# Kernel optimization log

Hardware: AMD Instinct MI355X
Metric: run time of the kernel (lower is better)

The kernel has to match this reference:

```python
import jax, jax.numpy as jnp
import numpy as np

IMAGE_W = 1024; IMAGE_H = 1024
STRIDES = (8, 16, 32, 64, 128)
TOP_N = 1000; MIN_SCORE = 0.01; NMS_THR = 0.6; MAX_DET = 100
BATCH = 16; NUM_CLASSES = 80


def setup_inputs():
    keys = jax.random.split(jax.random.key(0), 3 * len(STRIDES))
    inp = {}
    for l, s in enumerate(STRIDES):
        H, W = IMAGE_H // s, IMAGE_W // s
        inp[f"cls_head_{l}"] = jax.random.normal(keys[3 * l], (BATCH, H, W, NUM_CLASSES), jnp.float32)
        inp[f"reg_head_{l}"] = jax.random.normal(keys[3 * l + 1], (BATCH, H, W, 4), jnp.float32)
        inp[f"center_head_{l}"] = jax.random.normal(keys[3 * l + 2], (BATCH, H, W, 1), jnp.float32)
        xs = (jnp.arange(W, dtype=jnp.float32) + 0.5) * s
        ys = (jnp.arange(H, dtype=jnp.float32) + 0.5) * s
        gx, gy = jnp.meshgrid(xs, ys)  # each [H, W]
        pos = jnp.stack([gx, gy], axis=-1)  # [H, W, 2] = (ctr_x, ctr_y)
        inp[f"position_{l}"] = jnp.broadcast_to(pos, (BATCH, H, W, 2))
    return inp


def _decode_levels(cls_heads, reg_heads, center_heads, positions):
    S, C, R, P = [], [], [], []
    for cls, reg, ctr, pos in zip(cls_heads, reg_heads, center_heads, positions):
        B = cls.shape[0]
        cls = jax.nn.sigmoid(cls).reshape(B, -1, cls.shape[-1])  # [B,N,C]
        reg = jnp.exp(reg).reshape(B, -1, 4)
        ctr = jax.nn.sigmoid(ctr).reshape(B, -1)
        pos = pos.reshape(B, -1, 2)
        scores = jnp.sqrt(jnp.max(cls, axis=2) * ctr)  # sqrt(cls_max * centerness)
        classes = jnp.argmax(cls, axis=2)
        if scores.shape[1] >= TOP_N:
            scores, idx = jax.lax.top_k(scores, TOP_N)
            classes = jnp.take_along_axis(classes, idx, axis=1)
            reg = jnp.take_along_axis(reg, idx[:, :, None], axis=1)
            pos = jnp.take_along_axis(pos, idx[:, :, None], axis=1)
        S.append(scores); C.append(classes); R.append(reg); P.append(pos)
    return (jnp.concatenate(S, 1), jnp.concatenate(C, 1),
            jnp.concatenate(R, 1), jnp.concatenate(P, 1))


def _nms_keep(boxes, valid, iou_thr):
    # greedy class-agnostic NMS on score-descending boxes [N,4]
    N = boxes.shape[0]
    x1, y1, x2, y2 = boxes[:, 0], boxes[:, 1], boxes[:, 2], boxes[:, 3]
    areas = (x2 - x1) * (y2 - y1)
    idx = jnp.arange(N)

    def body(i, suppressed):
        keep_i = valid[i] & ~suppressed[i]
        xx1 = jnp.maximum(x1[i], x1); yy1 = jnp.maximum(y1[i], y1)
        xx2 = jnp.minimum(x2[i], x2); yy2 = jnp.minimum(y2[i], y2)
        inter = jnp.maximum(xx2 - xx1, 0.0) * jnp.maximum(yy2 - yy1, 0.0)
        iou = inter / (areas[i] + areas - inter)
        return suppressed | (keep_i & (iou > iou_thr) & (idx > i))

    suppressed = jax.lax.fori_loop(0, N, body, jnp.zeros((N,), bool))
    return valid & ~suppressed


def _per_image(scores, classes, reg, pos):
    xy_min = pos - reg[:, 0:2]
    xy_max = pos + reg[:, 2:4]
    boxes = jnp.concatenate([xy_min, xy_max], axis=1).astype(jnp.int32)  # trunc like .int()
    boxes = jnp.stack([jnp.maximum(boxes[:, 0], 0),
                       jnp.maximum(boxes[:, 1], 0),
                       jnp.minimum(boxes[:, 2], IMAGE_W - 1),
                       jnp.minimum(boxes[:, 3], IMAGE_H - 1)], axis=1).astype(jnp.float32)
    valid = scores > MIN_SCORE
    order = jnp.argsort(jnp.where(valid, -scores, jnp.inf))  # valid, score-descending first
    sb, ss = boxes[order], scores[order]
    sc, sv = classes[order].astype(jnp.float32), valid[order]
    kept = _nms_keep(sb, sv, NMS_THR)
    rank = jnp.cumsum(kept) - 1
    slot = jnp.where(kept, jnp.minimum(rank, MAX_DET), MAX_DET)  # overflow -> scratch slot
    out_s = jnp.full((MAX_DET + 1,), -1.0, jnp.float32).at[slot].set(jnp.where(kept, ss, -1.0))[:MAX_DET]
    out_c = jnp.full((MAX_DET + 1,), -1.0, jnp.float32).at[slot].set(jnp.where(kept, sc, -1.0))[:MAX_DET]
    out_b = jnp.full((MAX_DET + 1, 4), -1.0, jnp.float32).at[slot].set(jnp.where(kept[:, None], sb, -1.0))[:MAX_DET]
    return out_s, out_c, out_b


def _forward(cls_heads, reg_heads, center_heads, positions):
    s, c, r, p = _decode_levels(cls_heads, reg_heads, center_heads, positions)
    return jax.vmap(_per_image)(s, c, r, p)


def reference(cls_head_0, reg_head_0, center_head_0, position_0,
              cls_head_1, reg_head_1, center_head_1, position_1,
              cls_head_2, reg_head_2, center_head_2, position_2,
              cls_head_3, reg_head_3, center_head_3, position_3,
              cls_head_4, reg_head_4, center_head_4, position_4):
    cls_heads = [cls_head_0, cls_head_1, cls_head_2, cls_head_3, cls_head_4]
    reg_heads = [reg_head_0, reg_head_1, reg_head_2, reg_head_3, reg_head_4]
    center_heads = [center_head_0, center_head_1, center_head_2, center_head_3, center_head_4]
    positions = [position_0, position_1, position_2, position_3, position_4]
    return _forward(cls_heads, reg_heads, center_heads, positions)
```

## Files before the change

kernel.cpp:

```cpp
#include <hip/hip_runtime.h>
#include <stdint.h>

#define BATCH 16
#define NCLS 80
#define NPOS 21824
#define POOLN 3320
#define MAXDET 100

#define CAP0 4096
#define CAP1 2432
#define CAP2 1024
#define C34 320
#define CAP34 320
#define SEG1 (CAP0)
#define SEG2 (CAP0 + CAP1)
#define SEG3 (CAP0 + CAP1 + CAP2)
#define CAPTOT (SEG3 + CAP34)

#define DEC_BPI 341
#define GATHER_BPI 16
#define GATHER_CHUNK 1344
#define POS_BPI 13

#define NBINS 4096
#define HIST_TPI 11

__device__ const int d_lvl_off[5] = {0, 16384, 20480, 21504, 21760};
__device__ const int d_lvl_hw[5]  = {16384, 4096, 1024, 256, 64};

struct Ptrs { const float* p[20]; };

__device__ __forceinline__ void map_lvl(int r, int& level, int& hw) {
  if      (r < 16384) { level = 0; hw = r; }
  else if (r < 20480) { level = 1; hw = r - 16384; }
  else if (r < 21504) { level = 2; hw = r - 20480; }
  else if (r < 21760) { level = 3; hw = r - 21504; }
  else                { level = 4; hw = r - 21760; }
}


__global__ __launch_bounds__(256) void decode_kernel(Ptrs args, uint4* __restrict__ dec,
                                                     unsigned long long* __restrict__ gbuf,
                                                     int* __restrict__ gcnt,
                                                     unsigned* __restrict__ sbuf) {
  __shared__ float2 sm[1280];
  int b  = blockIdx.x / DEC_BPI;
  int bb = blockIdx.x - b * DEC_BPI;
  int t = threadIdx.x;
  if (bb == 0 && t < 3) gcnt[b * 3 + t] = 0;

  int flat0 = bb * 64;
  int level, hw0;
  map_lvl(flat0, level, hw0);
  int HW = d_lvl_hw[level];

  const float* cls = args.p[level * 4 + 0];
  const float* reg = args.p[level * 4 + 1];
  const float* ctr = args.p[level * 4 + 2];
  const float* pos = args.p[level * 4 + 3];

  const float4* c4 = (const float4*)(cls + ((long)b * HW + hw0) * NCLS);
#pragma unroll
  for (int w = 0; w < 5; ++w) {
    int f = t + 256 * w;
    float4 v = c4[f];
    int q = f % 20;
    float m = -1e30f; int am = 4 * q;
    if (v.x > m) { m = v.x; am = 4 * q + 0; }
    if (v.y > m) { m = v.y; am = 4 * q + 1; }
    if (v.z > m) { m = v.z; am = 4 * q + 2; }
    if (v.w > m) { m = v.w; am = 4 * q + 3; }
    sm[f] = make_float2(m, __int_as_float(am));
  }
  __syncthreads();

  int aoff = t >> 2, r = t & 3;
  int base = aoff * 20 + 5 * r;
  float2 c0 = sm[base];
  float m = c0.x; int am = __float_as_int(c0.y);
#pragma unroll
  for (int i = 1; i < 5; ++i) {
    float2 cc = sm[base + i];
    int oa = __float_as_int(cc.y);
    if (cc.x > m || (cc.x == m && oa < am)) { m = cc.x; am = oa; }
  }
#pragma unroll
  for (int d = 1; d <= 2; d <<= 1) {
    float om = __shfl_xor(m, d, 64);
    int   oa = __shfl_xor(am, d, 64);
    if (om > m || (om == m && oa < am)) { m = om; am = oa; }
  }

  if (r == 0) {
    int hw = hw0 + aoff;
    long abase = (long)b * HW + hw;
    float4 rg = *(const float4*)(reg + abase * 4);
    float  ct = ctr[abase];
    float2 ps = ((const float2*)pos)[abase];

    float e0 = expf(rg.x), e1 = expf(rg.y), e2 = expf(rg.z), e3 = expf(rg.w);
    int x1 = (int)(ps.x - e0);
    int y1 = (int)(ps.y - e1);
    int x2 = (int)(ps.x + e2);
    int y2 = (int)(ps.y + e3);
    x1 = max(x1, 0); y1 = max(y1, 0);
    x2 = min(x2, 1023); y2 = min(y2, 1023);

    float sigm = 1.0f / (1.0f + expf(-m));
    float sigc = 1.0f / (1.0f + expf(-ct));
    float score = sqrtf(sigm * sigc);

    uint4 e;
    e.x = __float_as_uint(score);
    e.y = (unsigned)am;
    e.z = (unsigned)(x1 & 0xFFFF) | ((unsigned)y1 << 16);
    e.w = (unsigned)(x2 & 0xFFFF) | ((unsigned)y2 << 16);
    dec[b * NPOS + flat0 + aoff] = e;

    unsigned nsb = ~e.x;
    sbuf[b * NPOS + flat0 + aoff] = nsb;
    if (level >= 3) {
      unsigned long long key =
          ((unsigned long long)nsb << 32) | (unsigned)((level << 20) | hw);
      gbuf[(size_t)b * CAPTOT + SEG3 + ((level == 3) ? hw : 256 + hw)] = key;
    }
  }
}

__global__ __launch_bounds__(256) void hist_kernel(const unsigned* __restrict__ sbuf,
                                                   unsigned* __restrict__ ghist) {
  __shared__ unsigned h[NBINS];
  int img = blockIdx.x / HIST_TPI, task = blockIdx.x % HIST_TPI;
  int level, start, n;
  if      (task < 8)  { level = 0; start = task * 2048;       n = 2048; }
  else if (task < 10) { level = 1; start = (task - 8) * 2048; n = 2048; }
  else                { level = 2; start = 0;                 n = 1024; }
  int tid = threadIdx.x;

  for (int i = tid; i < NBINS; i += 256) h[i] = 0;
  __syncthreads();
  const unsigned* base = sbuf + img * NPOS + d_lvl_off[level] + start;
  for (int i = tid; i < n; i += 256)
    atomicAdd(&h[base[i] >> 20], 1u);
  __syncthreads();
  unsigned* gh = ghist + (unsigned)(img * 3 + level) * NBINS;
  for (int i = tid; i < NBINS; i += 256) {
    unsigned v = h[i];
    if (v) atomicAdd(&gh[i], v);
  }
}

__global__ __launch_bounds__(256) void cutoff_kernel(const unsigned* __restrict__ ghist,
                                                     int* __restrict__ bcut) {
  __shared__ unsigned wpart[4];
  __shared__ int shB;
  int img = blockIdx.x / 3, level = blockIdx.x % 3;
  const unsigned* h = ghist + (unsigned)(img * 3 + level) * NBINS;
  int tid = threadIdx.x, lane = tid & 63, wv = tid >> 6;

  unsigned hl[16];
  unsigned s = 0;
#pragma unroll
  for (int k = 0; k < 16; ++k) { hl[k] = h[16 * tid + k]; s += hl[k]; }
  unsigned incl = s;
  for (int d = 1; d < 64; d <<= 1) {
    unsigned v = __shfl_up(incl, d, 64);
    if (lane >= d) incl += v;
  }
  if (lane == 63) wpart[wv] = incl;
  __syncthreads();
  unsigned woff = 0;
  for (int w = 0; w < wv; ++w) woff += wpart[w];
  unsigned excl = woff + incl - s;
  if (excl < 1000u && excl + s >= 1000u) {
    unsigned cum = excl; int B = NBINS - 1;
#pragma unroll
    for (int k = 0; k < 16; ++k) {
      cum += hl[k];
      if (cum >= 1000u) { B = 16 * tid + k; break; }
    }
    shB = B;
  }
  __syncthreads();
  if (tid == 0) bcut[img * 3 + level] = shB;
}

__global__ __launch_bounds__(256) void gather_kernel(const unsigned* __restrict__ sbuf,
                                                     const int* __restrict__ bcut,
                                                     unsigned long long* __restrict__ gbuf,
                                                     int* __restrict__ gcnt) {
  int img = blockIdx.x / GATHER_BPI, bb = blockIdx.x % GATHER_BPI;
  int tid = threadIdx.x, lane = tid & 63;
  int start = bb * GATHER_CHUNK;
  int b0 = bcut[img * 3 + 0], b1 = bcut[img * 3 + 1], b2 = bcut[img * 3 + 2];
  unsigned long long* gb = gbuf + (size_t)img * CAPTOT;

  for (int j = start + tid; j < start + GATHER_CHUNK; j += 256) {
    int level, hw;
    map_lvl(j, level, hw);
    unsigned nsb = sbuf[img * NPOS + j];
    bool sel = (int)(nsb >> 20) <= ((level == 0) ? b0 : (level == 1) ? b1 : b2);
    unsigned long long msk = __ballot(sel);
    if (msk) {
      int nsel = __popcll(msk);
      int bas = 0;
      if (lane == 0) bas = atomicAdd(&gcnt[img * 3 + level], nsel);
      bas = __shfl(bas, 0, 64);
      if (sel) {
        int p = bas + __popcll(msk & ((1ULL << lane) - 1ULL));
        int cap   = (level == 0) ? CAP0 : (level == 1) ? CAP1 : CAP2;
        int sbase = (level == 0) ? 0    : (level == 1) ? SEG1 : SEG2;
        unsigned long long key =
            ((unsigned long long)nsb << 32) | (unsigned)((level << 20) | hw);
        if (p < cap) gb[sbase + p] = key;
      }
    }
  }
}

#define SWQ(q) ((q) ^ (((q) >> 3) & 7))

__device__ __forceinline__ void cmpswap(unsigned long long& a, unsigned long long& b,
                                        bool asc) {
  unsigned long long mn = a < b ? a : b;
  unsigned long long mx = a < b ? b : a;
  a = asc ? mn : mx;
  b = asc ? mx : mn;
}

__global__ __launch_bounds__(256) void sort_kernel(unsigned long long* __restrict__ gbuf,
                                                   const int* __restrict__ gcnt) {
  __shared__ ulonglong2 lds2[2048];
  int img = blockIdx.x >> 2, sg = blockIdx.x & 3;
  int t = threadIdx.x;
  unsigned long long* gb = gbuf + (size_t)img * CAPTOT;

  int base, cap;
  if      (sg == 0) { base = 0;    cap = CAP0; }
  else if (sg == 1) { base = SEG1; cap = CAP1; }
  else if (sg == 2) { base = SEG2; cap = CAP2; }
  else              { base = SEG3; cap = C34;  }
  int c = (sg < 3) ? min(gcnt[img * 3 + sg], cap) : C34;

  int Pnet = 512;
  while (Pnet < c) Pnet <<= 1;

  for (int q = t; q < (Pnet >> 1); q += 256) {
    int e0 = 2 * q;
    ulonglong2 val;
    val.x = (e0     < c) ? gb[base + e0]     : ~0ULL;
    val.y = (e0 + 1 < c) ? gb[base + e0 + 1] : ~0ULL;
    lds2[SWQ(q)] = val;
  }
  __syncthreads();

  unsigned long long key[16];
  if (t * 16 < Pnet) {
#pragma unroll
    for (int w = 0; w < 8; ++w) {
      ulonglong2 val = lds2[SWQ(t * 8 + w)];
      key[2 * w]     = val.x;
      key[2 * w + 1] = val.y;
    }
  } else {
#pragma unroll
    for (int v = 0; v < 16; ++v) key[v] = ~0ULL;
  }

#pragma unroll
  for (int kk = 2; kk <= 8; kk <<= 1)
#pragma unroll
    for (int j = kk >> 1; j >= 1; j >>= 1)
#pragma unroll
      for (int v = 0; v < 16; ++v)
        if (!(v & j)) cmpswap(key[v], key[v | j], (v & kk) == 0);

  for (int k = 16; k <= Pnet; k <<= 1) {
    bool asc = (t & (k >> 4)) == 0;
    for (int j = k >> 1; j >= 16; j >>= 1) {
      int d = j >> 4;
      bool keep_min = ((t & d) == 0) == asc;
      if (d <= 32) {
#pragma unroll
        for (int v = 0; v < 16; ++v) {
          unsigned long long p = __shfl_xor(key[v], d, 64);
          unsigned long long mn = key[v] < p ? key[v] : p;
          unsigned long long mx = key[v] < p ? p : key[v];
          key[v] = keep_min ? mn : mx;
        }
      } else {
        __syncthreads();
#pragma unroll
        for (int w = 0; w < 8; ++w)
          lds2[SWQ(t * 8 + w)] = make_ulonglong2(key[2 * w], key[2 * w + 1]);
        __syncthreads();
        int tp = t ^ d;
#pragma unroll
        for (int w = 0; w < 8; ++w) {
          ulonglong2 pv = lds2[SWQ(tp * 8 + w)];
          unsigned long long a = key[2 * w], b = key[2 * w + 1];
          unsigned long long mn0 = a < pv.x ? a : pv.x, mx0 = a < pv.x ? pv.x : a;
          unsigned long long mn1 = b < pv.y ? b : pv.y, mx1 = b < pv.y ? pv.y : b;
          key[2 * w]     = keep_min ? mn0 : mx0;
          key[2 * w + 1] = keep_min ? mn1 : mx1;
        }
      }
    }
#pragma unroll
    for (int j = 8; j >= 1; j >>= 1)
#pragma unroll
      for (int v = 0; v < 16; ++v)
        if (!(v & j)) cmpswap(key[v], key[v | j], asc);
  }

  __syncthreads();
  if (t * 16 < Pnet) {
#pragma unroll
    for (int w = 0; w < 8; ++w)
      lds2[SWQ(t * 8 + w)] = make_ulonglong2(key[2 * w], key[2 * w + 1]);
  }
  __syncthreads();
  int npairs = (c + 1) >> 1;
  ulonglong2* gb2 = (ulonglong2*)(gb + base);
  for (int q = t; q < npairs; q += 256) gb2[q] = lds2[SWQ(q)];
}

__device__ __forceinline__ int lbound(const unsigned long long* __restrict__ a,
                                      int n, unsigned long long x) {
  int lo = 0, len = n;
  while (len > 0) {
    int half = len >> 1;
    int mid = lo + half;
    if (a[mid] < x) { lo = mid + 1; len -= half + 1; }
    else            { len = half; }
  }
  return lo;
}

__global__ __launch_bounds__(256) void pos_kernel(const unsigned long long* __restrict__ gbuf,
                                                  const int* __restrict__ gcnt,
                                                  unsigned long long* __restrict__ pool) {
  int img = blockIdx.x / POS_BPI, bb = blockIdx.x % POS_BPI;
  int e = bb * 256 + threadIdx.x;
  const unsigned long long* gb = gbuf + (size_t)img * CAPTOT;

  int c0 = min(gcnt[img * 3 + 0], CAP0);
  int c1 = min(gcnt[img * 3 + 1], CAP1);
  int c2 = min(gcnt[img * 3 + 2], CAP2);
  int m0 = min(c0, 1000), m1 = min(c1, 1000), m2 = min(c2, 1000);
  int tot = m0 + m1 + m2 + C34;
  if (e >= tot) return;

  int t, i;
  if      (e < m0)           { t = 0; i = e; }
  else if (e < m0 + m1)      { t = 1; i = e - m0; }
  else if (e < m0 + m1 + m2) { t = 2; i = e - m0 - m1; }
  else                       { t = 3; i = e - m0 - m1 - m2; }

  const int off[4] = {0, SEG1, SEG2, SEG3};
  const int cc[4]  = {c0, c1, c2, C34};

  unsigned long long key = gb[off[t] + i];
  int pos = i;
#pragma unroll
  for (int u = 0; u < 4; ++u) {
    if (u == t) continue;
    pos += min(lbound(gb + off[u], cc[u], key), 1000);
  }
  pool[img * POOLN + pos] = key;
}

__global__ __launch_bounds__(64) void nms_kernel(const uint4* __restrict__ dec,
                                                 const unsigned long long* __restrict__ pool,
                                                 float* __restrict__ out) {
  __shared__ int4 kbox[MAXDET];
  __shared__ int  karea[MAXDET];
  int img = blockIdx.x;
  int lane = threadIdx.x;

  float* out_s = out + img * MAXDET;
  float* out_c = out + BATCH * MAXDET + img * MAXDET;
  float* out_b = out + 2 * BATCH * MAXDET + img * MAXDET * 4;

  int k = 0;
  bool full = false;

  for (int b0 = 0; b0 < POOLN; b0 += 64) {
    int i = b0 + lane;
    bool inb = i < POOLN;

    float sc = -1.0f;
    int4 bx = make_int4(0, 0, 0, 0);
    int ar = 0;
    unsigned cls = 0;
    if (inb) {
      unsigned long long key = pool[img * POOLN + i];
      unsigned low = (unsigned)key;
      int level = (low >> 20) & 7;
      int idx = low & 0xFFFFF;
      uint4 e = dec[img * NPOS + d_lvl_off[level] + idx];
      sc = __uint_as_float(e.x);
      cls = e.y;
      bx = make_int4((int)(e.z & 0xFFFF), (int)(e.z >> 16),
                     (int)(e.w & 0xFFFF), (int)(e.w >> 16));
      ar = (bx.z - bx.x) * (bx.w - bx.y);
    }

    bool invalid = !(sc > 0.01f);
    if (__all(invalid)) break;
    bool sup = invalid;

    for (int t = 0; t < k; ++t) {
      int4 kb = kbox[t];
      int  ka = karea[t];
      int xx1 = max(bx.x, kb.x), yy1 = max(bx.y, kb.y);
      int xx2 = min(bx.z, kb.z), yy2 = min(bx.w, kb.w);
      int iw = max(xx2 - xx1, 0), ih = max(yy2 - yy1, 0);
      int inter = iw * ih;
      int uni = ar + ka - inter;
      sup = sup || (((long long)inter << 25) > 20132661LL * (long long)uni);
    }

    unsigned long long alive = __ballot(!sup);
    while (alive) {
      int j = __ffsll(alive) - 1;

      int jx1 = __shfl(bx.x, j, 64), jy1 = __shfl(bx.y, j, 64);
      int jx2 = __shfl(bx.z, j, 64), jy2 = __shfl(bx.w, j, 64);
      int ja  = __shfl(ar,   j, 64);

      if (lane == j) {
        kbox[k]  = bx;
        karea[k] = ar;
        out_s[k] = sc;
        out_c[k] = (float)(int)cls;
        out_b[k * 4 + 0] = (float)bx.x;
        out_b[k * 4 + 1] = (float)bx.y;
        out_b[k * 4 + 2] = (float)bx.z;
        out_b[k * 4 + 3] = (float)bx.w;
      }
      ++k;
      if (k == MAXDET) { full = true; break; }

      if (lane > j) {
        int xx1 = max(bx.x, jx1), yy1 = max(bx.y, jy1);
        int xx2 = min(bx.z, jx2), yy2 = min(bx.w, jy2);
        int iw = max(xx2 - xx1, 0), ih = max(yy2 - yy1, 0);
        int inter = iw * ih;
        int uni = ar + ja - inter;
        sup = sup || (((long long)inter << 25) > 20132661LL * (long long)uni);
      }

      unsigned long long himask = (j < 63) ? (~0ULL << (j + 1)) : 0ULL;
      alive = __ballot(!sup) & himask;
    }
    if (full) break;
  }

  for (int s = k + lane; s < MAXDET; s += 64) {
    out_s[s] = -1.0f;
    out_c[s] = -1.0f;
    out_b[s * 4 + 0] = -1.0f;
    out_b[s * 4 + 1] = -1.0f;
    out_b[s * 4 + 2] = -1.0f;
    out_b[s * 4 + 3] = -1.0f;
  }
}

extern "C" void kernel_launch(void* const* d_in, const int* in_sizes, int n_in,
                              void* d_out, int out_size, void* d_ws, size_t ws_size,
                              hipStream_t stream) {
  Ptrs args;
  for (int i = 0; i < 20; ++i) args.p[i] = (const float*)d_in[i];

  char* ws = (char*)d_ws;
  uint4* dec = (uint4*)ws;
  ws += (size_t)BATCH * NPOS * 16;
  unsigned long long* pool = (unsigned long long*)ws;
  ws += (size_t)BATCH * POOLN * 8;
  unsigned long long* gbuf = (unsigned long long*)ws;
  ws += (size_t)BATCH * CAPTOT * 8;
  unsigned* sbuf = (unsigned*)ws;
  ws += (size_t)BATCH * NPOS * 4;
  unsigned* ghist = (unsigned*)ws;
  ws += (size_t)BATCH * 3 * NBINS * 4;
  int* gcnt = (int*)ws;
  ws += 192;
  int* bcut = (int*)ws;
  float* out = (float*)d_out;

  hipMemsetAsync(ghist, 0, (size_t)BATCH * 3 * NBINS * 4, stream);

  decode_kernel<<<BATCH * DEC_BPI, 256, 0, stream>>>(args, dec, gbuf, gcnt, sbuf);
  hist_kernel<<<BATCH * HIST_TPI, 256, 0, stream>>>(sbuf, ghist);
  cutoff_kernel<<<BATCH * 3, 256, 0, stream>>>(ghist, bcut);
  gather_kernel<<<BATCH * GATHER_BPI, 256, 0, stream>>>(sbuf, bcut, gbuf, gcnt);
  sort_kernel<<<BATCH * 4, 256, 0, stream>>>(gbuf, gcnt);
  pos_kernel<<<BATCH * POS_BPI, 256, 0, stream>>>(gbuf, gcnt, pool);
  nms_kernel<<<BATCH, 64, 0, stream>>>(dec, pool, out);
}
```

Baseline: 312.8 us.

## Fuse histogram, cutoff, gather and sort into one per-segment kernel

Merges the hist, cutoff, gather and sort kernels into a single selectsort kernel. Each block builds the histogram in shared memory, finds the top-1000 cutoff bin, compacts the selected keys straight into LDS, then sorts them. This drops the memset, three launches and the global histogram and candidate round trips. The cost is less parallelism: one block per level per image (64 blocks) now scans up to 16384 entries that were previously spread over many blocks, and the compaction order now comes from a shared-memory atomic counter instead of a global one.

```diff
diff --git a/kernel.cpp b/kernel.cpp
--- a/kernel.cpp
+++ b/kernel.cpp
@@ -11,19 +11,14 @@
 #define CAP1 2432
 #define CAP2 1024
 #define C34 320
-#define CAP34 320
 #define SEG1 (CAP0)
 #define SEG2 (CAP0 + CAP1)
 #define SEG3 (CAP0 + CAP1 + CAP2)
-#define CAPTOT (SEG3 + CAP34)
+#define CAPTOT (SEG3 + C34)
 
 #define DEC_BPI 341
-#define GATHER_BPI 16
-#define GATHER_CHUNK 1344
 #define POS_BPI 13
-
 #define NBINS 4096
-#define HIST_TPI 11
 
 __device__ const int d_lvl_off[5] = {0, 16384, 20480, 21504, 21760};
 __device__ const int d_lvl_hw[5]  = {16384, 4096, 1024, 256, 64};
@@ -41,13 +36,11 @@
 
 __global__ __launch_bounds__(256) void decode_kernel(Ptrs args, uint4* __restrict__ dec,
                                                      unsigned long long* __restrict__ gbuf,
-                                                     int* __restrict__ gcnt,
                                                      unsigned* __restrict__ sbuf) {
   __shared__ float2 sm[1280];
   int b  = blockIdx.x / DEC_BPI;
   int bb = blockIdx.x - b * DEC_BPI;
   int t = threadIdx.x;
-  if (bb == 0 && t < 3) gcnt[b * 3 + t] = 0;
 
   int flat0 = bb * 64;
   int level, hw0;
@@ -127,98 +120,8 @@
   }
 }
 
-__global__ __launch_bounds__(256) void hist_kernel(const unsigned* __restrict__ sbuf,
-                                                   unsigned* __restrict__ ghist) {
-  __shared__ unsigned h[NBINS];
-  int img = blockIdx.x / HIST_TPI, task = blockIdx.x % HIST_TPI;
-  int level, start, n;
-  if      (task < 8)  { level = 0; start = task * 2048;       n = 2048; }
-  else if (task < 10) { level = 1; start = (task - 8) * 2048; n = 2048; }
-  else                { level = 2; start = 0;                 n = 1024; }
-  int tid = threadIdx.x;
-
-  for (int i = tid; i < NBINS; i += 256) h[i] = 0;
-  __syncthreads();
-  const unsigned* base = sbuf + img * NPOS + d_lvl_off[level] + start;
-  for (int i = tid; i < n; i += 256)
-    atomicAdd(&h[base[i] >> 20], 1u);
-  __syncthreads();
-  unsigned* gh = ghist + (unsigned)(img * 3 + level) * NBINS;
-  for (int i = tid; i < NBINS; i += 256) {
-    unsigned v = h[i];
-    if (v) atomicAdd(&gh[i], v);
-  }
-}
-
-__global__ __launch_bounds__(256) void cutoff_kernel(const unsigned* __restrict__ ghist,
-                                                     int* __restrict__ bcut) {
-  __shared__ unsigned wpart[4];
-  __shared__ int shB;
-  int img = blockIdx.x / 3, level = blockIdx.x % 3;
-  const unsigned* h = ghist + (unsigned)(img * 3 + level) * NBINS;
-  int tid = threadIdx.x, lane = tid & 63, wv = tid >> 6;
-
-  unsigned hl[16];
-  unsigned s = 0;
-#pragma unroll
-  for (int k = 0; k < 16; ++k) { hl[k] = h[16 * tid + k]; s += hl[k]; }
-  unsigned incl = s;
-  for (int d = 1; d < 64; d <<= 1) {
-    unsigned v = __shfl_up(incl, d, 64);
-    if (lane >= d) incl += v;
-  }
-  if (lane == 63) wpart[wv] = incl;
-  __syncthreads();
-  unsigned woff = 0;
-  for (int w = 0; w < wv; ++w) woff += wpart[w];
-  unsigned excl = woff + incl - s;
-  if (excl < 1000u && excl + s >= 1000u) {
-    unsigned cum = excl; int B = NBINS - 1;
-#pragma unroll
-    for (int k = 0; k < 16; ++k) {
-      cum += hl[k];
-      if (cum >= 1000u) { B = 16 * tid + k; break; }
-    }
-    shB = B;
-  }
-  __syncthreads();
-  if (tid == 0) bcut[img * 3 + level] = shB;
-}
-
-__global__ __launch_bounds__(256) void gather_kernel(const unsigned* __restrict__ sbuf,
-                                                     const int* __restrict__ bcut,
-                                                     unsigned long long* __restrict__ gbuf,
-                                                     int* __restrict__ gcnt) {
-  int img = blockIdx.x / GATHER_BPI, bb = blockIdx.x % GATHER_BPI;
-  int tid = threadIdx.x, lane = tid & 63;
-  int start = bb * GATHER_CHUNK;
-  int b0 = bcut[img * 3 + 0], b1 = bcut[img * 3 + 1], b2 = bcut[img * 3 + 2];
-  unsigned long long* gb = gbuf + (size_t)img * CAPTOT;
-
-  for (int j = start + tid; j < start + GATHER_CHUNK; j += 256) {
-    int level, hw;
-    map_lvl(j, level, hw);
-    unsigned nsb = sbuf[img * NPOS + j];
-    bool sel = (int)(nsb >> 20) <= ((level == 0) ? b0 : (level == 1) ? b1 : b2);
-    unsigned long long msk = __ballot(sel);
-    if (msk) {
-      int nsel = __popcll(msk);
-      int bas = 0;
-      if (lane == 0) bas = atomicAdd(&gcnt[img * 3 + level], nsel);
-      bas = __shfl(bas, 0, 64);
-      if (sel) {
-        int p = bas + __popcll(msk & ((1ULL << lane) - 1ULL));
-        int cap   = (level == 0) ? CAP0 : (level == 1) ? CAP1 : CAP2;
-        int sbase = (level == 0) ? 0    : (level == 1) ? SEG1 : SEG2;
-        unsigned long long key =
-            ((unsigned long long)nsb << 32) | (unsigned)((level << 20) | hw);
-        if (p < cap) gb[sbase + p] = key;
-      }
-    }
-  }
-}
-
 #define SWQ(q) ((q) ^ (((q) >> 3) & 7))
+#define LKI(e) (2 * SWQ((e) >> 1) + ((e) & 1))
 
 __device__ __forceinline__ void cmpswap(unsigned long long& a, unsigned long long& b,
                                         bool asc) {
@@ -228,32 +131,93 @@
   b = asc ? mx : mn;
 }
 
-__global__ __launch_bounds__(256) void sort_kernel(unsigned long long* __restrict__ gbuf,
-                                                   const int* __restrict__ gcnt) {
-  __shared__ ulonglong2 lds2[2048];
+__global__ __launch_bounds__(256) void selectsort_kernel(const unsigned* __restrict__ sbuf,
+                                                         unsigned long long* __restrict__ gbuf,
+                                                         int* __restrict__ gcnt) {
+  __shared__ unsigned h[NBINS];
+  __shared__ unsigned long long lk[4096];
+  __shared__ unsigned wpart[4];
+  __shared__ int shB;
+  __shared__ int sh_cnt;
+
   int img = blockIdx.x >> 2, sg = blockIdx.x & 3;
-  int t = threadIdx.x;
+  int t = threadIdx.x, lane = t & 63, wv = t >> 6;
   unsigned long long* gb = gbuf + (size_t)img * CAPTOT;
 
-  int base, cap;
-  if      (sg == 0) { base = 0;    cap = CAP0; }
-  else if (sg == 1) { base = SEG1; cap = CAP1; }
-  else if (sg == 2) { base = SEG2; cap = CAP2; }
-  else              { base = SEG3; cap = C34;  }
-  int c = (sg < 3) ? min(gcnt[img * 3 + sg], cap) : C34;
+  int base, cap, n, loff;
+  if      (sg == 0) { base = 0;    cap = CAP0; n = 16384; loff = 0; }
+  else if (sg == 1) { base = SEG1; cap = CAP1; n = 4096;  loff = 16384; }
+  else if (sg == 2) { base = SEG2; cap = CAP2; n = 1024;  loff = 20480; }
+  else              { base = SEG3; cap = C34;  n = 0;     loff = 0; }
+
+  int c;
+  if (sg < 3) {
+    for (int i = t; i < NBINS; i += 256) h[i] = 0;
+    if (t == 0) sh_cnt = 0;
+    __syncthreads();
+    const unsigned* sb = sbuf + img * NPOS + loff;
+    for (int i = t; i < n; i += 256) atomicAdd(&h[sb[i] >> 20], 1u);
+    __syncthreads();
+
+    unsigned hl[16]; unsigned s = 0;
+#pragma unroll
+    for (int k = 0; k < 16; ++k) { hl[k] = h[16 * t + k]; s += hl[k]; }
+    unsigned incl = s;
+    for (int d = 1; d < 64; d <<= 1) {
+      unsigned v = __shfl_up(incl, d, 64);
+      if (lane >= d) incl += v;
+    }
+    if (lane == 63) wpart[wv] = incl;
+    __syncthreads();
+    unsigned woff = 0;
+    for (int w = 0; w < wv; ++w) woff += wpart[w];
+    unsigned excl = woff + incl - s;
+    if (excl < 1000u && excl + s >= 1000u) {
+      unsigned cum = excl; int B = NBINS - 1;
+#pragma unroll
+      for (int k = 0; k < 16; ++k) {
+        cum += hl[k];
+        if (cum >= 1000u) { B = 16 * t + k; break; }
+      }
+      shB = B;
+    }
+    __syncthreads();
+    int B = shB;
+
+    for (int i = t; i < n; i += 256) {
+      unsigned nsb = sb[i];
+      bool sel = (int)(nsb >> 20) <= B;
+      unsigned long long msk = __ballot(sel);
+      if (msk) {
+        int nsel = __popcll(msk);
+        int bas = 0;
+        if (lane == 0) bas = atomicAdd(&sh_cnt, nsel);
+        bas = __shfl(bas, 0, 64);
+        if (sel) {
+          int p = bas + __popcll(msk & ((1ULL << lane) - 1ULL));
+          if (p < cap) {
+            unsigned long long key =
+                ((unsigned long long)nsb << 32) | (unsigned)((sg << 20) | i);
+            lk[LKI(p)] = key;
+          }
+        }
+      }
+    }
+    __syncthreads();
+    c = min(sh_cnt, cap);
+    if (t == 0) gcnt[img * 3 + sg] = sh_cnt;
+  } else {
+    for (int i = t; i < C34; i += 256) lk[LKI(i)] = gb[SEG3 + i];
+    c = C34;
+    __syncthreads();
+  }
 
   int Pnet = 512;
   while (Pnet < c) Pnet <<= 1;
-
-  for (int q = t; q < (Pnet >> 1); q += 256) {
-    int e0 = 2 * q;
-    ulonglong2 val;
-    val.x = (e0     < c) ? gb[base + e0]     : ~0ULL;
-    val.y = (e0 + 1 < c) ? gb[base + e0 + 1] : ~0ULL;
-    lds2[SWQ(q)] = val;
-  }
+  for (int e = c + t; e < Pnet; e += 256) lk[LKI(e)] = ~0ULL;
   __syncthreads();
 
+  ulonglong2* lds2 = (ulonglong2*)lk;
   unsigned long long key[16];
   if (t * 16 < Pnet) {
 #pragma unroll
@@ -482,20 +446,11 @@
   ws += (size_t)BATCH * CAPTOT * 8;
   unsigned* sbuf = (unsigned*)ws;
   ws += (size_t)BATCH * NPOS * 4;
-  unsigned* ghist = (unsigned*)ws;
-  ws += (size_t)BATCH * 3 * NBINS * 4;
   int* gcnt = (int*)ws;
-  ws += 192;
-  int* bcut = (int*)ws;
   float* out = (float*)d_out;
 
-  hipMemsetAsync(ghist, 0, (size_t)BATCH * 3 * NBINS * 4, stream);
-
-  decode_kernel<<<BATCH * DEC_BPI, 256, 0, stream>>>(args, dec, gbuf, gcnt, sbuf);
-  hist_kernel<<<BATCH * HIST_TPI, 256, 0, stream>>>(sbuf, ghist);
-  cutoff_kernel<<<BATCH * 3, 256, 0, stream>>>(ghist, bcut);
-  gather_kernel<<<BATCH * GATHER_BPI, 256, 0, stream>>>(sbuf, bcut, gbuf, gcnt);
-  sort_kernel<<<BATCH * 4, 256, 0, stream>>>(gbuf, gcnt);
+  decode_kernel<<<BATCH * DEC_BPI, 256, 0, stream>>>(args, dec, gbuf, sbuf);
+  selectsort_kernel<<<BATCH * 4, 256, 0, stream>>>(sbuf, gbuf, gcnt);
   pos_kernel<<<BATCH * POS_BPI, 256, 0, stream>>>(gbuf, gcnt, pool);
   nms_kernel<<<BATCH, 64, 0, stream>>>(dec, pool, out);
 }
```

Measured after the change: 308.4 us. About the same (-1.4%).
